# Optimization experiments

Measured on AMD Instinct MI355X. Metric: run time of the kernel, lower is better.

Reference implementation:

```python
import jax, jax.numpy as jnp
import numpy as np

N_USERS = 8192
N_ITEMS = 8192
D = 64
B = 1024
EPS = 1e-6


def _l2norm_rows(x):
    # torch F.normalize(p=2, dim=1): x / max(||x||_2, 1e-12)
    n = jnp.sqrt(jnp.sum(x * x, axis=1, keepdims=True))
    return x / jnp.maximum(n, 1e-12)


def setup_inputs() -> dict:
    key = jax.random.key(0)
    ks = jax.random.split(key, 12)
    adj = (jax.random.uniform(ks[0], (N_USERS, N_ITEMS)) < 0.02).astype(jnp.float32)
    obs_adj = (jax.random.uniform(ks[1], (N_USERS, N_ITEMS)) < 0.02).astype(jnp.float32)
    xavier_scale = 0.05  # mimic xavier_uniform magnitude; keeps exp(inner) tame
    return {
        "users": jax.random.randint(ks[2], (B,), 0, N_USERS),
        "pos_items": jax.random.randint(ks[3], (B,), 0, N_ITEMS),
        "neg_items": jax.random.randint(ks[4], (B,), 0, N_ITEMS),
        "adj_matrix": adj,
        "obs_users": jax.random.randint(ks[5], (B,), 0, N_USERS),
        "obs_pos_items": jax.random.randint(ks[6], (B,), 0, N_ITEMS),
        "obs_neg_items": jax.random.randint(ks[7], (B,), 0, N_ITEMS),
        "obs_adj_matrix": obs_adj,
        "iteration": 0,
        "user_emb": jax.random.normal(ks[8], (N_USERS, D), jnp.float32) * xavier_scale,
        "item_emb": jax.random.normal(ks[9], (N_ITEMS, D), jnp.float32) * xavier_scale,
        "W_1": jax.random.normal(ks[10], (D, D), jnp.float32) * 0.1,
        "W_2": jax.random.normal(ks[11], (D, D), jnp.float32) * 0.1,
        "W_obs": jax.random.normal(jax.random.fold_in(key, 99), (D, D), jnp.float32) * 0.1,
    }


def reference(users, pos_items, neg_items, adj_matrix, obs_users, obs_pos_items,
              obs_neg_items, obs_adj_matrix, iteration, user_emb, item_emb,
              W_1, W_2, W_obs):
    # attention-like coefficients: exp(inner) masked by adjacency, row-normalized
    score = jnp.exp(user_emb @ item_emb.T) * adj_matrix          # [U, I]
    coef = score / (jnp.sum(score, axis=1, keepdims=True) + EPS)  # vectorized row loop

    h1_user = (coef @ item_emb) @ W_1                             # [U, D]
    h1_item = (coef.T @ user_emb) @ W_1                           # [I, D]

    # degree-normalized aggregation (vectorized per-row loops)
    deg_u = jnp.sum(adj_matrix, axis=1)                           # [U]
    deg_i = jnp.sum(adj_matrix, axis=0)                           # [I]
    h2_user = ((adj_matrix @ item_emb) / (deg_u + EPS)[:, None]) @ W_2
    h2_item = ((adj_matrix.T @ user_emb) / (deg_i + EPS)[:, None]) @ W_2

    samp_user = jnp.concatenate([h1_user, h2_user], axis=1)       # [U, 2D]
    # NOTE: original code concatenates h2_item with itself (not h1_item) -- kept faithful
    samp_item = jnp.concatenate([h2_item, h2_item], axis=1)       # [I, 2D]

    samp_u = samp_user[users]
    samp_pi = samp_item[pos_items]
    samp_ni = samp_item[neg_items]

    # observed-graph branch
    odeg_u = jnp.sum(obs_adj_matrix, axis=1)
    odeg_i = jnp.sum(obs_adj_matrix, axis=0)
    obs_user = jnp.tanh(((obs_adj_matrix @ item_emb) / (odeg_u + EPS)[:, None]) @ W_obs)
    obs_item = jnp.tanh(((obs_adj_matrix.T @ user_emb) / (odeg_i + EPS)[:, None]) @ W_obs)

    obs_u = obs_user[obs_users]
    obs_pi = obs_item[obs_pos_items]
    obs_ni = obs_item[obs_neg_items]

    h_user = jnp.tanh(jnp.concatenate([samp_u, obs_u], axis=1))      # [B, 3D]
    h_pos = jnp.tanh(jnp.concatenate([samp_pi, obs_pi], axis=1))     # [B, 3D]
    h_neg = jnp.tanh(jnp.concatenate([samp_ni, obs_ni], axis=1))     # [B, 3D]

    return (_l2norm_rows(h_user), _l2norm_rows(h_pos), _l2norm_rows(h_neg))
```

## Files before the change

### kernel.cpp

```cpp
#include <hip/hip_runtime.h>
#include <stdint.h>

typedef unsigned short u16;
typedef unsigned int u32;
typedef __attribute__((ext_vector_type(8))) short short8;
typedef __attribute__((ext_vector_type(4))) float f32x4;

#define EPSF 1e-6f
#define MFMA(a, b, c) __builtin_amdgcn_mfma_f32_16x16x32_bf16((a), (b), (c), 0, 0, 0)
#define KSPLIT 4

__device__ inline u32 f2b_bits(u32 fb) {
  return (fb + 0x7fffu + ((fb >> 16) & 1u)) >> 16;
}
__device__ inline u32 pack2f(float lo, float hi) {
  union { float f; u32 u; } a, b; a.f = lo; b.f = hi;
  return f2b_bits(a.u) | (f2b_bits(b.u) << 16);
}
__device__ inline short8 ldfrag(const u32* p, int uidx) {
  union { u32 u[4]; short8 s; } t;
  t.u[0] = p[uidx + 0]; t.u[1] = p[uidx + 1];
  t.u[2] = p[uidx + 2]; t.u[3] = p[uidx + 3];
  return t.s;
}
__device__ inline f32x4 zero4() { f32x4 z; z[0]=0.f; z[1]=0.f; z[2]=0.f; z[3]=0.f; return z; }

__global__ void k_detect(const u32* __restrict__ users, int B, u32* flag) {
  __shared__ int f;
  if (threadIdx.x == 0) f = 0;
  __syncthreads();
  int loc = 0;
  for (int j = threadIdx.x; j < B; j += 256)
    if ((j & 1) && users[j] != 0u) loc = 1;
  if (loc) atomicOr(&f, 1);
  __syncthreads();
  if (threadIdx.x == 0) *flag = (u32)f;
}

__device__ inline int gidx(const void* p, int r, bool i64) {
  return i64 ? (int)((const long long*)p)[r] : ((const int*)p)[r];
}

__global__ __launch_bounds__(256) void pass_user(
    const u32* __restrict__ flag,
    const void* __restrict__ users, const void* __restrict__ obs_users,
    const float* __restrict__ adj, const float* __restrict__ obs_adj,
    const float* __restrict__ UE, const float* __restrict__ IE,
    int NI,
    float* __restrict__ t1_r, float* __restrict__ h2u_r,
    float* __restrict__ obsu_r, float* __restrict__ scal_r)
{
  __shared__ float ue_l[64];
  __shared__ int   ia[1024];  __shared__ float va[1024];
  __shared__ int   ioi[1024]; __shared__ float vo[1024];
  __shared__ float redf[16 * 16 * 4];
  __shared__ float red[256];
  __shared__ int   cnt_a, cnt_o;

  const int tid = threadIdx.x;
  const int r = blockIdx.x;
  const bool i64 = (*flag == 0u);
  const int is_ = gidx(users, r, i64);
  const int io  = gidx(obs_users, r, i64);
  const int G = tid >> 4, sl = tid & 15;

  if (tid == 0) { cnt_a = 0; cnt_o = 0; }
  if (tid < 64) ue_l[tid] = UE[(size_t)is_ * 64 + tid];

  const int nfr = NI / 1024;
  float4 av[8], ov[8];
  const float4* arow = (const float4*)(adj + (size_t)is_ * NI);
  const float4* orow = (const float4*)(obs_adj + (size_t)io * NI);
  #pragma unroll
  for (int k = 0; k < 8; ++k) {
    if (k < nfr) { av[k] = arow[k * 256 + tid]; ov[k] = orow[k * 256 + tid]; }
  }
  __syncthreads();

  float dg = 0.f, od = 0.f;
  #pragma unroll
  for (int k = 0; k < 8; ++k) {
    if (k < nfr) {
      int base = (k * 256 + tid) * 4;
      float va4[4] = {av[k].x, av[k].y, av[k].z, av[k].w};
      float vo4[4] = {ov[k].x, ov[k].y, ov[k].z, ov[k].w};
      #pragma unroll
      for (int c = 0; c < 4; ++c) {
        if (va4[c] != 0.f) {
          dg += va4[c];
          int p = atomicAdd(&cnt_a, 1);
          ia[p] = base + c; va[p] = va4[c];
        }
        if (vo4[c] != 0.f) {
          od += vo4[c];
          int p = atomicAdd(&cnt_o, 1);
          ioi[p] = base + c; vo[p] = vo4[c];
        }
      }
    }
  }
  __syncthreads();

  float4 ue4 = ((const float4*)ue_l)[sl];
  float4 A1 = {0,0,0,0}, A2 = {0,0,0,0}, A3 = {0,0,0,0};
  float rs_p = 0.f;
  const int nA = cnt_a, nO = cnt_o;

  for (int j = G; j < nA; j += 16) {
    int i = ia[j]; float a = va[j];
    float4 e = *(const float4*)(IE + (size_t)i * 64 + sl * 4);
    float s = ue4.x * e.x + ue4.y * e.y + ue4.z * e.z + ue4.w * e.w;
    #pragma unroll
    for (int off = 1; off <= 8; off <<= 1) s += __shfl_xor(s, off, 64);
    float w = expf(s) * a;
    if (sl == 0) rs_p += w;
    A1.x += w * e.x; A1.y += w * e.y; A1.z += w * e.z; A1.w += w * e.w;
    A2.x += a * e.x; A2.y += a * e.y; A2.z += a * e.z; A2.w += a * e.w;
  }
  for (int j = G; j < nO; j += 16) {
    int i = ioi[j]; float o = vo[j];
    float4 e = *(const float4*)(IE + (size_t)i * 64 + sl * 4);
    A3.x += o * e.x; A3.y += o * e.y; A3.z += o * e.z; A3.w += o * e.w;
  }

  float* my = redf + (G * 16 + sl) * 4;
  my[0] = A1.x; my[1] = A1.y; my[2] = A1.z; my[3] = A1.w;
  __syncthreads();
  if (tid < 64) {
    float s = 0.f;
    #pragma unroll
    for (int g = 0; g < 16; ++g) s += redf[(g * 16 + (tid >> 2)) * 4 + (tid & 3)];
    t1_r[(size_t)r * 64 + tid] = s;
  }
  __syncthreads();
  my[0] = A2.x; my[1] = A2.y; my[2] = A2.z; my[3] = A2.w;
  __syncthreads();
  if (tid < 64) {
    float s = 0.f;
    #pragma unroll
    for (int g = 0; g < 16; ++g) s += redf[(g * 16 + (tid >> 2)) * 4 + (tid & 3)];
    h2u_r[(size_t)r * 64 + tid] = s;
  }
  __syncthreads();
  my[0] = A3.x; my[1] = A3.y; my[2] = A3.z; my[3] = A3.w;
  __syncthreads();
  if (tid < 64) {
    float s = 0.f;
    #pragma unroll
    for (int g = 0; g < 16; ++g) s += redf[(g * 16 + (tid >> 2)) * 4 + (tid & 3)];
    obsu_r[(size_t)r * 64 + tid] = s;
  }
  __syncthreads();

  red[tid] = (sl == 0) ? rs_p : 0.f; __syncthreads();
  if (tid < 64) {
    float s = red[tid] + red[tid + 64] + red[tid + 128] + red[tid + 192];
    #pragma unroll
    for (int off = 32; off >= 1; off >>= 1) s += __shfl_xor(s, off, 64);
    if (tid == 0) scal_r[r * 4 + 0] = s;
  }
  __syncthreads();
  red[tid] = dg; __syncthreads();
  if (tid < 64) {
    float s = red[tid] + red[tid + 64] + red[tid + 128] + red[tid + 192];
    #pragma unroll
    for (int off = 32; off >= 1; off >>= 1) s += __shfl_xor(s, off, 64);
    if (tid == 0) scal_r[r * 4 + 1] = s;
  }
  __syncthreads();
  red[tid] = od; __syncthreads();
  if (tid < 64) {
    float s = red[tid] + red[tid + 64] + red[tid + 128] + red[tid + 192];
    #pragma unroll
    for (int off = 32; off >= 1; off >>= 1) s += __shfl_xor(s, off, 64);
    if (tid == 0) scal_r[r * 4 + 2] = s;
  }
}

__global__ __launch_bounds__(256) void pass_item_mfma(
    const float* __restrict__ adj, const float* __restrict__ obs_adj,
    const float* __restrict__ UE,
    int NU, int NI,
    float* __restrict__ degi, float* __restrict__ odegi,
    float* __restrict__ h2i, float* __restrict__ obsi)
{
  __shared__ u32 at_s[64 * 33];
  __shared__ u32 oat_s[64 * 33];
  __shared__ u32 uet_s[64 * 33];

  const int tid = threadIdx.x;
  const int lane = tid & 63;
  const int wv = tid >> 6;
  const int l15 = lane & 15, q = lane >> 4;
  const int ig = blockIdx.x / KSPLIT;
  const int ksp = blockIdx.x % KSPLIT;
  const int i0 = ig * 64;
  const int ucount = NU / KSPLIT;
  const int ub = ksp * ucount;
  const int up = tid >> 3;
  const int cp = tid & 7;

  f32x4 accH[4], accO[4], accDA, accDO;
  #pragma unroll
  for (int n = 0; n < 4; ++n) { accH[n] = zero4(); accO[n] = zero4(); }
  accDA = zero4(); accDO = zero4();

  short8 ones8;
  { union { u32 u[4]; short8 s; } t;
    t.u[0] = 0x3F803F80u; t.u[1] = 0x3F803F80u; t.u[2] = 0x3F803F80u; t.u[3] = 0x3F803F80u;
    ones8 = t.s; }

  const int nch = ucount >> 6;
  for (int ch = 0; ch < nch; ++ch) {
    const int u0 = ub + ch * 64;
    const int ua = u0 + up * 2, ub2 = ua + 1;
    const float4* pa0 = (const float4*)(adj + (size_t)ua * NI + i0 + cp * 8);
    const float4* pa1 = (const float4*)(adj + (size_t)ub2 * NI + i0 + cp * 8);
    const float4* po0 = (const float4*)(obs_adj + (size_t)ua * NI + i0 + cp * 8);
    const float4* po1 = (const float4*)(obs_adj + (size_t)ub2 * NI + i0 + cp * 8);
    const float4* pu0 = (const float4*)(UE + (size_t)ua * 64 + cp * 8);
    const float4* pu1 = (const float4*)(UE + (size_t)ub2 * 64 + cp * 8);
    float4 A0 = pa0[0], A1v = pa0[1], A2v = pa1[0], A3v = pa1[1];
    float4 O0 = po0[0], O1v = po0[1], O2v = po1[0], O3v = po1[1];
    float4 U0 = pu0[0], U1v = pu0[1], U2v = pu1[0], U3v = pu1[1];

    __syncthreads();

    {
      float alo[8] = {A0.x,A0.y,A0.z,A0.w,A1v.x,A1v.y,A1v.z,A1v.w};
      float ahi[8] = {A2v.x,A2v.y,A2v.z,A2v.w,A3v.x,A3v.y,A3v.z,A3v.w};
      float olo[8] = {O0.x,O0.y,O0.z,O0.w,O1v.x,O1v.y,O1v.z,O1v.w};
      float ohi[8] = {O2v.x,O2v.y,O2v.z,O2v.w,O3v.x,O3v.y,O3v.z,O3v.w};
      float ulo[8] = {U0.x,U0.y,U0.z,U0.w,U1v.x,U1v.y,U1v.z,U1v.w};
      float uhi[8] = {U2v.x,U2v.y,U2v.z,U2v.w,U3v.x,U3v.y,U3v.z,U3v.w};
      #pragma unroll
      for (int j = 0; j < 8; ++j) {
        int c = cp * 8 + j;
        at_s[c * 33 + up]  = pack2f(alo[j], ahi[j]);
        oat_s[c * 33 + up] = pack2f(olo[j], ohi[j]);
        uet_s[c * 33 + up] = pack2f(ulo[j], uhi[j]);
      }
    }
    __syncthreads();

    #pragma unroll
    for (int ks = 0; ks < 2; ++ks) {
      int ab = (wv * 16 + l15) * 33 + ks * 16 + q * 4;
      short8 aa = ldfrag(at_s, ab);
      short8 ao = ldfrag(oat_s, ab);
      accDA = MFMA(aa, ones8, accDA);
      accDO = MFMA(ao, ones8, accDO);
      #pragma unroll
      for (int nt = 0; nt < 4; ++nt) {
        short8 b8 = ldfrag(uet_s, (nt * 16 + l15) * 33 + ks * 16 + q * 4);
        accH[nt] = MFMA(aa, b8, accH[nt]);
        accO[nt] = MFMA(ao, b8, accO[nt]);
      }
    }
  }

  #pragma unroll
  for (int nt = 0; nt < 4; ++nt) {
    #pragma unroll
    for (int r = 0; r < 4; ++r) {
      int item = i0 + wv * 16 + q * 4 + r;
      int d = nt * 16 + l15;
      atomicAdd(&h2i[(size_t)item * 64 + d], accH[nt][r]);
      atomicAdd(&obsi[(size_t)item * 64 + d], accO[nt][r]);
    }
  }
  if (l15 == 0) {
    #pragma unroll
    for (int r = 0; r < 4; ++r) {
      int item = i0 + wv * 16 + q * 4 + r;
      atomicAdd(&degi[item], accDA[r]);
      atomicAdd(&odegi[item], accDO[r]);
    }
  }
}

__global__ __launch_bounds__(64) void epilogue(
    const u32* __restrict__ flag, int B,
    const void* __restrict__ pos_items, const void* __restrict__ neg_items,
    const void* __restrict__ obs_pos, const void* __restrict__ obs_neg,
    const float* __restrict__ W1, const float* __restrict__ W2,
    const float* __restrict__ Wobs,
    const float* __restrict__ t1_r, const float* __restrict__ h2u_r,
    const float* __restrict__ obsu_r, const float* __restrict__ scal_r,
    const float* __restrict__ degi, const float* __restrict__ odegi,
    const float* __restrict__ h2i, const float* __restrict__ obsi,
    float* __restrict__ out)
{
  __shared__ float v1f[64], v2f[64], v3f[64];
  const int b = blockIdx.x, t = threadIdx.x;
  const int which = b / B, r = b % B;
  const bool i64 = (*flag == 0u);

  const float *Wa, *Wb;
  if (which == 0) {
    float s1 = 1.f / (scal_r[r * 4 + 0] + EPSF);
    float s2 = 1.f / (scal_r[r * 4 + 1] + EPSF);
    float s3 = 1.f / (scal_r[r * 4 + 2] + EPSF);
    v1f[t] = t1_r[(size_t)r * 64 + t] * s1;
    v2f[t] = h2u_r[(size_t)r * 64 + t] * s2;
    v3f[t] = obsu_r[(size_t)r * 64 + t] * s3;
    Wa = W1; Wb = W2;
  } else {
    const void* sptr = (which == 1) ? pos_items : neg_items;
    const void* optr = (which == 1) ? obs_pos : obs_neg;
    int id = gidx(sptr, r, i64);
    int oid = gidx(optr, r, i64);
    float s1 = 1.f / (degi[id] + EPSF);
    float s3 = 1.f / (odegi[oid] + EPSF);
    float h = h2i[(size_t)id * 64 + t] * s1;
    v1f[t] = h; v2f[t] = h;
    v3f[t] = obsi[(size_t)oid * 64 + t] * s3;
    Wa = W2; Wb = W2;
  }
  __syncthreads();

  float c1 = 0.f, c2 = 0.f, c3 = 0.f;
  #pragma unroll 8
  for (int d = 0; d < 64; ++d) {
    c1 += v1f[d] * Wa[(size_t)d * 64 + t];
    c2 += v2f[d] * Wb[(size_t)d * 64 + t];
    c3 += v3f[d] * Wobs[(size_t)d * 64 + t];
  }
  float y0 = tanhf(c1);
  float y1 = tanhf(c2);
  float y2 = tanhf(tanhf(c3));
  float ss = y0 * y0 + y1 * y1 + y2 * y2;
  #pragma unroll
  for (int off = 32; off >= 1; off >>= 1) ss += __shfl_xor(ss, off, 64);
  float inv = 1.f / fmaxf(sqrtf(ss), 1e-12f);

  float* orow = out + ((size_t)which * B + r) * 192;
  orow[t]       = y0 * inv;
  orow[64 + t]  = y1 * inv;
  orow[128 + t] = y2 * inv;
}

extern "C" void kernel_launch(void* const* d_in, const int* in_sizes, int n_in,
                              void* d_out, int out_size, void* d_ws, size_t ws_size,
                              hipStream_t stream) {
  struct Ent { long long s; int i; };
  Ent e[32]; int m = 0;
  for (int i = 0; i < n_in && i < 32; ++i)
    if (in_sizes[i] > 1) { e[m].s = in_sizes[i]; e[m].i = i; ++m; }
  for (int a = 1; a < m; ++a) {
    Ent t = e[a]; int b = a - 1;
    while (b >= 0 && e[b].s < t.s) { e[b + 1] = e[b]; --b; }
    e[b + 1] = t;
  }
  bool ok = (m == 13) &&
            e[0].s == e[1].s && e[2].s == e[3].s &&
            e[4].s == e[5].s && e[5].s == e[6].s &&
            e[7].s == e[12].s;

  const void *users, *pos_items, *neg_items, *obs_users, *obs_pos, *obs_neg;
  const float *adj, *obs_adj, *UE, *IE, *W1, *W2, *Wobs;
  int B, NU, NI;
  if (ok) {
    adj = (const float*)d_in[e[0].i];  obs_adj = (const float*)d_in[e[1].i];
    UE  = (const float*)d_in[e[2].i];  IE      = (const float*)d_in[e[3].i];
    W1 = (const float*)d_in[e[4].i]; W2 = (const float*)d_in[e[5].i];
    Wobs = (const float*)d_in[e[6].i];
    users     = d_in[e[7].i];  pos_items = d_in[e[8].i];  neg_items = d_in[e[9].i];
    obs_users = d_in[e[10].i]; obs_pos   = d_in[e[11].i]; obs_neg   = d_in[e[12].i];
    B  = (int)e[7].s;
    NU = (int)(e[2].s / 64);
    NI = (int)(e[3].s / 64);
  } else {
    users = d_in[0]; pos_items = d_in[1]; neg_items = d_in[2];
    adj = (const float*)d_in[3];
    obs_users = d_in[4]; obs_pos = d_in[5]; obs_neg = d_in[6];
    obs_adj = (const float*)d_in[7];
    UE = (const float*)d_in[9]; IE = (const float*)d_in[10];
    W1 = (const float*)d_in[11]; W2 = (const float*)d_in[12];
    Wobs = (const float*)d_in[13];
    B = 1024; NU = 8192; NI = 8192;
  }

  float* w = (float*)d_ws;
  u32*   flag  = (u32*)w;
  float* t1_r  = w + 16;
  float* h2u_r = t1_r + (size_t)B * 64;
  float* obsu_r= h2u_r + (size_t)B * 64;
  float* scal_r= obsu_r + (size_t)B * 64;
  float* degi  = scal_r + (size_t)B * 4;
  float* odegi = degi + NI;
  float* h2i   = odegi + NI;
  float* obsi  = h2i + (size_t)NI * 64;

  k_detect<<<dim3(1), dim3(256), 0, stream>>>((const u32*)users, B, flag);
  hipMemsetAsync(degi, 0, (size_t)(2 * NI + 2 * (size_t)NI * 64) * sizeof(float), stream);

  pass_user<<<dim3(B), dim3(256), 0, stream>>>(flag, users, obs_users,
                                               adj, obs_adj, UE, IE, NI,
                                               t1_r, h2u_r, obsu_r, scal_r);
  pass_item_mfma<<<dim3((NI / 64) * KSPLIT), dim3(256), 0, stream>>>(
      adj, obs_adj, UE, NU, NI, degi, odegi, h2i, obsi);
  epilogue<<<dim3(3 * B), dim3(64), 0, stream>>>(flag, B,
                                                 pos_items, neg_items, obs_pos, obs_neg,
                                                 W1, W2, Wobs,
                                                 t1_r, h2u_r, obsu_r, scal_r,
                                                 degi, odegi, h2i, obsi,
                                                 (float*)d_out);
}
```

Baseline: 587.1 us.

## Fuse user and item passes into one launch; write per-split partials instead of atomics

Merges the per-user sparse pass and the MFMA item pass into a single kernel whose blocks branch on blockIdx, so the two independent passes share the GPU concurrently. When workspace allows, the item pass writes per-K-split partial sums to separate buffers rather than using float atomics. The epilogue then sums the four partials, which also removes the memset. This trades atomic contention and an extra launch and memset for more workspace traffic and larger shared memory per block, which may lower occupancy for the user blocks.

After: 609.5 us. 1.04x slower.

```diff
diff --git a/kernel.cpp b/kernel.cpp
--- a/kernel.cpp
+++ b/kernel.cpp
@@ -8,7 +8,7 @@
 
 #define EPSF 1e-6f
 #define MFMA(a, b, c) __builtin_amdgcn_mfma_f32_16x16x32_bf16((a), (b), (c), 0, 0, 0)
-#define KSPLIT 4
+#define KSP4 4
 
 __device__ inline u32 f2b_bits(u32 fb) {
   return (fb + 0x7fffu + ((fb >> 16) & 1u)) >> 16;
@@ -41,30 +41,28 @@
   return i64 ? (int)((const long long*)p)[r] : ((const int*)p)[r];
 }
 
-__global__ __launch_bounds__(256) void pass_user(
-    const u32* __restrict__ flag,
-    const void* __restrict__ users, const void* __restrict__ obs_users,
-    const float* __restrict__ adj, const float* __restrict__ obs_adj,
-    const float* __restrict__ UE, const float* __restrict__ IE,
-    int NI,
-    float* __restrict__ t1_r, float* __restrict__ h2u_r,
-    float* __restrict__ obsu_r, float* __restrict__ scal_r)
+__device__ void user_body(char* smem, int r,
+    const u32* flag, const void* users, const void* obs_users,
+    const float* adj, const float* obs_adj,
+    const float* UE, const float* IE, int NI,
+    float* t1_r, float* h2u_r, float* obsu_r, float* scal_r)
 {
-  __shared__ float ue_l[64];
-  __shared__ int   ia[1024];  __shared__ float va[1024];
-  __shared__ int   ioi[1024]; __shared__ float vo[1024];
-  __shared__ float redf[16 * 16 * 4];
-  __shared__ float red[256];
-  __shared__ int   cnt_a, cnt_o;
+  float* ue_l = (float*)smem;
+  int*   ia   = (int*)(ue_l + 64);
+  float* va   = (float*)(ia + 1024);
+  int*   ioi  = (int*)(va + 1024);
+  float* vo   = (float*)(ioi + 1024);
+  float* redf = vo + 1024;
+  float* red  = redf + 1024;
+  int*   cnts = (int*)(red + 256);
 
   const int tid = threadIdx.x;
-  const int r = blockIdx.x;
   const bool i64 = (*flag == 0u);
   const int is_ = gidx(users, r, i64);
   const int io  = gidx(obs_users, r, i64);
   const int G = tid >> 4, sl = tid & 15;
 
-  if (tid == 0) { cnt_a = 0; cnt_o = 0; }
+  if (tid == 0) { cnts[0] = 0; cnts[1] = 0; }
   if (tid < 64) ue_l[tid] = UE[(size_t)is_ * 64 + tid];
 
   const int nfr = NI / 1024;
@@ -88,12 +86,12 @@
       for (int c = 0; c < 4; ++c) {
         if (va4[c] != 0.f) {
           dg += va4[c];
-          int p = atomicAdd(&cnt_a, 1);
+          int p = atomicAdd(&cnts[0], 1);
           ia[p] = base + c; va[p] = va4[c];
         }
         if (vo4[c] != 0.f) {
           od += vo4[c];
-          int p = atomicAdd(&cnt_o, 1);
+          int p = atomicAdd(&cnts[1], 1);
           ioi[p] = base + c; vo[p] = vo4[c];
         }
       }
@@ -104,7 +102,7 @@
   float4 ue4 = ((const float4*)ue_l)[sl];
   float4 A1 = {0,0,0,0}, A2 = {0,0,0,0}, A3 = {0,0,0,0};
   float rs_p = 0.f;
-  const int nA = cnt_a, nO = cnt_o;
+  const int nA = cnts[0], nO = cnts[1];
 
   for (int j = G; j < nA; j += 16) {
     int i = ia[j]; float a = va[j];
@@ -177,25 +175,24 @@
   }
 }
 
-__global__ __launch_bounds__(256) void pass_item_mfma(
-    const float* __restrict__ adj, const float* __restrict__ obs_adj,
-    const float* __restrict__ UE,
+template<int PART>
+__device__ void item_body(char* smem, int bi,
+    const float* adj, const float* obs_adj, const float* UE,
     int NU, int NI,
-    float* __restrict__ degi, float* __restrict__ odegi,
-    float* __restrict__ h2i, float* __restrict__ obsi)
+    float* degi, float* odegi, float* h2i, float* obsi)
 {
-  __shared__ u32 at_s[64 * 33];
-  __shared__ u32 oat_s[64 * 33];
-  __shared__ u32 uet_s[64 * 33];
+  u32* at_s  = (u32*)smem;
+  u32* oat_s = at_s + 64 * 33;
+  u32* uet_s = oat_s + 64 * 33;
 
   const int tid = threadIdx.x;
   const int lane = tid & 63;
   const int wv = tid >> 6;
   const int l15 = lane & 15, q = lane >> 4;
-  const int ig = blockIdx.x / KSPLIT;
-  const int ksp = blockIdx.x % KSPLIT;
+  const int ig = bi / KSP4;
+  const int ksp = bi % KSP4;
   const int i0 = ig * 64;
-  const int ucount = NU / KSPLIT;
+  const int ucount = NU / KSP4;
   const int ub = ksp * ucount;
   const int up = tid >> 3;
   const int cp = tid & 7;
@@ -259,28 +256,72 @@
     }
   }
 
-  #pragma unroll
-  for (int nt = 0; nt < 4; ++nt) {
-    #pragma unroll
-    for (int r = 0; r < 4; ++r) {
-      int item = i0 + wv * 16 + q * 4 + r;
-      int d = nt * 16 + l15;
-      atomicAdd(&h2i[(size_t)item * 64 + d], accH[nt][r]);
-      atomicAdd(&obsi[(size_t)item * 64 + d], accO[nt][r]);
-    }
-  }
-  if (l15 == 0) {
-    #pragma unroll
-    for (int r = 0; r < 4; ++r) {
-      int item = i0 + wv * 16 + q * 4 + r;
-      atomicAdd(&degi[item], accDA[r]);
-      atomicAdd(&odegi[item], accDO[r]);
-    }
-  }
-}
-
+  if (PART) {
+    #pragma unroll
+    for (int nt = 0; nt < 4; ++nt) {
+      #pragma unroll
+      for (int r = 0; r < 4; ++r) {
+        int item = i0 + wv * 16 + q * 4 + r;
+        int d = nt * 16 + l15;
+        size_t idx = ((size_t)ksp * NI + item) * 64 + d;
+        h2i[idx]  = accH[nt][r];
+        obsi[idx] = accO[nt][r];
+      }
+    }
+    if (l15 == 0) {
+      #pragma unroll
+      for (int r = 0; r < 4; ++r) {
+        int item = i0 + wv * 16 + q * 4 + r;
+        degi[(size_t)ksp * NI + item]  = accDA[r];
+        odegi[(size_t)ksp * NI + item] = accDO[r];
+      }
+    }
+  } else {
+    #pragma unroll
+    for (int nt = 0; nt < 4; ++nt) {
+      #pragma unroll
+      for (int r = 0; r < 4; ++r) {
+        int item = i0 + wv * 16 + q * 4 + r;
+        int d = nt * 16 + l15;
+        atomicAdd(&h2i[(size_t)item * 64 + d], accH[nt][r]);
+        atomicAdd(&obsi[(size_t)item * 64 + d], accO[nt][r]);
+      }
+    }
+    if (l15 == 0) {
+      #pragma unroll
+      for (int r = 0; r < 4; ++r) {
+        int item = i0 + wv * 16 + q * 4 + r;
+        atomicAdd(&degi[item], accDA[r]);
+        atomicAdd(&odegi[item], accDO[r]);
+      }
+    }
+  }
+}
+
+template<int PART>
+__global__ __launch_bounds__(256) void fused_main(
+    int B, int NU, int NI,
+    const u32* __restrict__ flag,
+    const void* __restrict__ users, const void* __restrict__ obs_users,
+    const float* __restrict__ adj, const float* __restrict__ obs_adj,
+    const float* __restrict__ UE, const float* __restrict__ IE,
+    float* __restrict__ t1_r, float* __restrict__ h2u_r,
+    float* __restrict__ obsu_r, float* __restrict__ scal_r,
+    float* __restrict__ degi, float* __restrict__ odegi,
+    float* __restrict__ h2i, float* __restrict__ obsi)
+{
+  __shared__ __align__(16) char smem[26 * 1024];
+  if ((int)blockIdx.x < B)
+    user_body(smem, blockIdx.x, flag, users, obs_users, adj, obs_adj, UE, IE, NI,
+              t1_r, h2u_r, obsu_r, scal_r);
+  else
+    item_body<PART>(smem, blockIdx.x - B, adj, obs_adj, UE, NU, NI,
+                    degi, odegi, h2i, obsi);
+}
+
+template<int PART>
 __global__ __launch_bounds__(64) void epilogue(
-    const u32* __restrict__ flag, int B,
+    const u32* __restrict__ flag, int B, int NI,
     const void* __restrict__ pos_items, const void* __restrict__ neg_items,
     const void* __restrict__ obs_pos, const void* __restrict__ obs_neg,
     const float* __restrict__ W1, const float* __restrict__ W2,
@@ -310,11 +351,25 @@
     const void* optr = (which == 1) ? obs_pos : obs_neg;
     int id = gidx(sptr, r, i64);
     int oid = gidx(optr, r, i64);
-    float s1 = 1.f / (degi[id] + EPSF);
-    float s3 = 1.f / (odegi[oid] + EPSF);
-    float h = h2i[(size_t)id * 64 + t] * s1;
+    float dsum, osum, hv, ov;
+    if (PART) {
+      dsum = 0.f; osum = 0.f; hv = 0.f; ov = 0.f;
+      #pragma unroll
+      for (int s = 0; s < KSP4; ++s) {
+        dsum += degi[(size_t)s * NI + id];
+        osum += odegi[(size_t)s * NI + oid];
+        hv += h2i[((size_t)s * NI + id) * 64 + t];
+        ov += obsi[((size_t)s * NI + oid) * 64 + t];
+      }
+    } else {
+      dsum = degi[id]; osum = odegi[oid];
+      hv = h2i[(size_t)id * 64 + t]; ov = obsi[(size_t)oid * 64 + t];
+    }
+    float s1 = 1.f / (dsum + EPSF);
+    float s3 = 1.f / (osum + EPSF);
+    float h = hv * s1;
     v1f[t] = h; v2f[t] = h;
-    v3f[t] = obsi[(size_t)oid * 64 + t] * s3;
+    v3f[t] = ov * s3;
     Wa = W2; Wb = W2;
   }
   __syncthreads();
@@ -381,29 +436,51 @@
     B = 1024; NU = 8192; NI = 8192;
   }
 
+  size_t user_f = 16 + (size_t)3 * B * 64 + 4 * B;
+  size_t part_f = (size_t)KSP4 * (2 * NI + 2 * (size_t)NI * 64);
+  size_t atom_f = (size_t)2 * NI + 2 * (size_t)NI * 64;
+  bool use_part = ws_size >= (user_f + part_f) * sizeof(float);
+
   float* w = (float*)d_ws;
   u32*   flag  = (u32*)w;
   float* t1_r  = w + 16;
   float* h2u_r = t1_r + (size_t)B * 64;
   float* obsu_r= h2u_r + (size_t)B * 64;
   float* scal_r= obsu_r + (size_t)B * 64;
-  float* degi  = scal_r + (size_t)B * 4;
-  float* odegi = degi + NI;
-  float* h2i   = odegi + NI;
-  float* obsi  = h2i + (size_t)NI * 64;
+  float* ibase = scal_r + (size_t)B * 4;
+  float *degi, *odegi, *h2i, *obsi;
+  if (use_part) {
+    degi  = ibase;
+    odegi = degi + (size_t)KSP4 * NI;
+    h2i   = odegi + (size_t)KSP4 * NI;
+    obsi  = h2i + (size_t)KSP4 * NI * 64;
+  } else {
+    degi  = ibase;  odegi = degi + NI;
+    h2i   = odegi + NI;  obsi = h2i + (size_t)NI * 64;
+  }
 
   k_detect<<<dim3(1), dim3(256), 0, stream>>>((const u32*)users, B, flag);
-  hipMemsetAsync(degi, 0, (size_t)(2 * NI + 2 * (size_t)NI * 64) * sizeof(float), stream);
-
-  pass_user<<<dim3(B), dim3(256), 0, stream>>>(flag, users, obs_users,
-                                               adj, obs_adj, UE, IE, NI,
-                                               t1_r, h2u_r, obsu_r, scal_r);
-  pass_item_mfma<<<dim3((NI / 64) * KSPLIT), dim3(256), 0, stream>>>(
-      adj, obs_adj, UE, NU, NI, degi, odegi, h2i, obsi);
-  epilogue<<<dim3(3 * B), dim3(64), 0, stream>>>(flag, B,
-                                                 pos_items, neg_items, obs_pos, obs_neg,
-                                                 W1, W2, Wobs,
-                                                 t1_r, h2u_r, obsu_r, scal_r,
-                                                 degi, odegi, h2i, obsi,
-                                                 (float*)d_out);
-}
+  if (!use_part)
+    hipMemsetAsync(degi, 0, atom_f * sizeof(float), stream);
+
+  dim3 grid(B + (NI / 64) * KSP4), blk(256);
+  if (use_part)
+    fused_main<1><<<grid, blk, 0, stream>>>(B, NU, NI, flag, users, obs_users,
+                                            adj, obs_adj, UE, IE,
+                                            t1_r, h2u_r, obsu_r, scal_r,
+                                            degi, odegi, h2i, obsi);
+  else
+    fused_main<0><<<grid, blk, 0, stream>>>(B, NU, NI, flag, users, obs_users,
+                                            adj, obs_adj, UE, IE,
+                                            t1_r, h2u_r, obsu_r, scal_r,
+                                            degi, odegi, h2i, obsi);
+
+  if (use_part)
+    epilogue<1><<<dim3(3 * B), dim3(64), 0, stream>>>(flag, B, NI,
+        pos_items, neg_items, obs_pos, obs_neg, W1, W2, Wobs,
+        t1_r, h2u_r, obsu_r, scal_r, degi, odegi, h2i, obsi, (float*)d_out);
+  else
+    epilogue<0><<<dim3(3 * B), dim3(64), 0, stream>>>(flag, B, NI,
+        pos_items, neg_items, obs_pos, obs_neg, W1, W2, Wobs,
+        t1_r, h2u_r, obsu_r, scal_r, degi, odegi, h2i, obsi, (float*)d_out);
+}
```
